# Kernel tuning notes

Hardware: AMD Instinct MI355X
Metric: run time of the kernel (lower is better)

The kernel has to match this reference:

```python
import jax, jax.numpy as jnp
import numpy as np

B, N, HID, NH = 8, 1024, 1024, 16
HD = HID // NH  # head_dim = 64
MLP = 4 * HID
EPS = 1e-6


def _xavier(key, fan_in, fan_out):
    lim = np.sqrt(6.0 / (fan_in + fan_out))
    return jax.random.uniform(key, (fan_in, fan_out), jnp.float32, -lim, lim)


def setup_inputs() -> dict:
    key = jax.random.key(0)
    ks = jax.random.split(key, 10)
    return {
        "x": jax.random.normal(ks[0], (B, N, HID), jnp.float32),
        "c": jax.random.normal(ks[1], (B, HID), jnp.float32),
        "w_ada": _xavier(ks[2], HID, 6 * HID), "b_ada": jnp.zeros((6 * HID,), jnp.float32),
        "wq": _xavier(ks[3], HID, HID), "bq": jnp.zeros((HID,), jnp.float32),
        "wk": _xavier(ks[4], HID, HID), "bk": jnp.zeros((HID,), jnp.float32),
        "wv": _xavier(ks[5], HID, HID), "bv": jnp.zeros((HID,), jnp.float32),
        "wo": _xavier(ks[6], HID, HID), "bo": jnp.zeros((HID,), jnp.float32),
        "w1": _xavier(ks[7], HID, MLP), "b1": jnp.zeros((MLP,), jnp.float32),
        "w2": _xavier(ks[8], MLP, HID), "b2": jnp.zeros((HID,), jnp.float32),
    }


def _ln(t):
    # LayerNorm, elementwise_affine=False, eps=1e-6
    mu = jnp.mean(t, axis=-1, keepdims=True)
    var = jnp.mean(jnp.square(t - mu), axis=-1, keepdims=True)
    return (t - mu) * jax.lax.rsqrt(var + EPS)


def _modulate(t, shift, scale):
    return t * (1.0 + scale[:, None, :]) + shift[:, None, :]


def reference(x, c, w_ada, b_ada, wq, bq, wk, bk, wv, bv, wo, bo, w1, b1, w2, b2):
    cmod = jax.nn.silu(c) @ w_ada + b_ada  # [B, 6*HID]
    sh_msa, sc_msa, g_msa, sh_mlp, sc_mlp, g_mlp = jnp.split(cmod, 6, axis=-1)

    xm = _modulate(_ln(x), sh_msa, sc_msa)  # [B, N, HID]
    q = (xm @ wq + bq).reshape(B, N, NH, HD)
    k = (xm @ wk + bk).reshape(B, N, NH, HD)
    v = (xm @ wv + bv).reshape(B, N, NH, HD)

    # NOTE: original scales by 1/head_dim (not 1/sqrt(head_dim)), fp32 softmax
    scores = jnp.einsum('bihd,bjhd->bhij', q, k) / HD
    attn = jax.nn.softmax(scores.astype(jnp.float32), axis=-1)
    out = jnp.einsum('bhij,bjhd->bihd', attn, v).astype(v.dtype)
    out = out.reshape(B, N, HID) @ wo + bo

    x = x + g_msa[:, None, :] * out

    xm2 = _modulate(_ln(x), sh_mlp, sc_mlp)
    h = jax.nn.gelu(xm2 @ w1 + b1, approximate=False)  # nn.GELU default = exact
    mlp_out = h @ w2 + b2
    return x + g_mlp[:, None, :] * mlp_out
```

## Files before the change

kernel.cpp:

```cpp
#include <hip/hip_runtime.h>
#include <hip/hip_bf16.h>
#include <cstdint>


typedef __bf16 bf16;
typedef __attribute__((ext_vector_type(8))) __bf16 bf16x8;
typedef __attribute__((ext_vector_type(4))) __bf16 bf16x4;
typedef __attribute__((ext_vector_type(4))) float f32x4;
typedef __attribute__((ext_vector_type(16))) float f32x16;

#define SEQ   1024
#define NHID  1024
#define NHEAD 16
#define HDIM  64
#define CMS   6144

#define GLD16(gp, lp)                                                  \
  __builtin_amdgcn_global_load_lds(                                    \
      (const __attribute__((address_space(1))) void*)(gp),             \
      (__attribute__((address_space(3))) void*)(lp), 16, 0, 0)

struct TP4 { const float* s[4]; bf16* d[4]; };

__global__ __launch_bounds__(256) void transpose_conv4(TP4 p)
{
  __shared__ float tile[32][33];
  const float* __restrict__ src = p.s[blockIdx.z];
  bf16* __restrict__ dst = p.d[blockIdx.z];
  int n0 = blockIdx.x * 32, k0 = blockIdx.y * 32;
  int tx = threadIdx.x & 31, ty = threadIdx.x >> 5;
#pragma unroll
  for (int i = 0; i < 32; i += 8)
    tile[ty + i][tx] = src[(size_t)(k0 + ty + i) * 1024 + n0 + tx];
  __syncthreads();
#pragma unroll
  for (int i = 0; i < 32; i += 8)
    dst[(size_t)(n0 + ty + i) * 1024 + k0 + tx] = (bf16)tile[tx][ty + i];
}

__global__ __launch_bounds__(256) void transpose_conv(
    const float* __restrict__ src, bf16* __restrict__ dst, int K, int N)
{
  __shared__ float tile[32][33];
  int n0 = blockIdx.x * 32, k0 = blockIdx.y * 32;
  int tx = threadIdx.x & 31, ty = threadIdx.x >> 5;
#pragma unroll
  for (int i = 0; i < 32; i += 8)
    tile[ty + i][tx] = src[(size_t)(k0 + ty + i) * N + n0 + tx];
  __syncthreads();
#pragma unroll
  for (int i = 0; i < 32; i += 8)
    dst[(size_t)(n0 + ty + i) * K + k0 + tx] = (bf16)tile[tx][ty + i];
}

__global__ __launch_bounds__(256) void ada_kernel(
    const float* __restrict__ c, const float* __restrict__ w_ada,
    const float* __restrict__ b_ada, float* __restrict__ cmod)
{
  __shared__ float cs[1024];
  int b = blockIdx.y;
  int col = blockIdx.x * 256 + threadIdx.x;
  for (int i = threadIdx.x; i < 1024; i += 256) {
    float cv = c[b * 1024 + i];
    cs[i] = cv / (1.0f + __expf(-cv));
  }
  __syncthreads();
  float acc = b_ada[col];
#pragma unroll 8
  for (int kk = 0; kk < 1024; kk++)
    acc += cs[kk] * w_ada[(size_t)kk * CMS + col];
  cmod[b * CMS + col] = acc;
}

__global__ __launch_bounds__(256) void ln_mod(
    const float* __restrict__ x, const float* __restrict__ cmod,
    bf16* __restrict__ out, int sh_off, int sc_off)
{
  int row = blockIdx.x, b = row >> 10, tid = threadIdx.x;
  const float4* xr = (const float4*)(x + (size_t)row * NHID);
  float4 v = xr[tid];
  float s  = v.x + v.y + v.z + v.w;
  float s2 = v.x * v.x + v.y * v.y + v.z * v.z + v.w * v.w;
#pragma unroll
  for (int off = 32; off; off >>= 1) {
    s  += __shfl_xor(s, off);
    s2 += __shfl_xor(s2, off);
  }
  __shared__ float red1[4], red2[4];
  int wave = tid >> 6, lane = tid & 63;
  if (lane == 0) { red1[wave] = s; red2[wave] = s2; }
  __syncthreads();
  float S  = red1[0] + red1[1] + red1[2] + red1[3];
  float S2 = red2[0] + red2[1] + red2[2] + red2[3];
  float mean = S * (1.0f / NHID);
  float var  = S2 * (1.0f / NHID) - mean * mean;
  float rs   = rsqrtf(var + 1e-6f);
  const float4* shp = (const float4*)(cmod + b * CMS + sh_off);
  const float4* scp = (const float4*)(cmod + b * CMS + sc_off);
  float4 sh4 = shp[tid], sc4 = scp[tid];
  bf16x4 o4;
  o4[0] = (bf16)((v.x - mean) * rs * (1.0f + sc4.x) + sh4.x);
  o4[1] = (bf16)((v.y - mean) * rs * (1.0f + sc4.y) + sh4.y);
  o4[2] = (bf16)((v.z - mean) * rs * (1.0f + sc4.z) + sh4.z);
  o4[3] = (bf16)((v.w - mean) * rs * (1.0f + sc4.w) + sh4.w);
  *(bf16x4*)(out + (size_t)row * NHID + tid * 4) = o4;
}

template <int EPI>
__global__ __launch_bounds__(256) void gemm_bt(
    const bf16* __restrict__ A, const bf16* __restrict__ Bt,
    const float* __restrict__ bias, const float* __restrict__ bias2,
    const float* __restrict__ bias3,
    bf16* __restrict__ outb, bf16* __restrict__ outb2,
    bf16* __restrict__ outb3, float* __restrict__ outf,
    const float* __restrict__ cmod, int gate_off,
    const float* __restrict__ resid,
    int N, int K)
{
  __shared__ __align__(16) bf16 As[128 * 64];
  __shared__ __align__(16) bf16 Bs[128 * 64];
  const int tid = threadIdx.x;
  const int bm = blockIdx.y * 128, bn = blockIdx.x * 128;

  const int wave = tid >> 6, lane = tid & 63;
  const int l32 = lane & 31, half = lane >> 5;
  const int wm = (wave >> 1) * 64, wn = (wave & 1) * 64;

  const int sr = tid >> 3;
  const int sc = tid & 7;

  f32x16 acc[2][2];
#pragma unroll
  for (int i = 0; i < 2; i++)
#pragma unroll
    for (int j = 0; j < 2; j++) acc[i][j] = (f32x16)0.0f;

  for (int k0 = 0; k0 < K; k0 += 64) {
#pragma unroll
    for (int i = 0; i < 4; i++) {
      int r = i * 32 + sr;
      int cg = (sc ^ (r & 7)) * 8;
      bf16* lbase_a = As + (size_t)(i * 256 + (tid & 192)) * 8;
      bf16* lbase_b = Bs + (size_t)(i * 256 + (tid & 192)) * 8;
      GLD16(A  + (size_t)(bm + r) * K + k0 + cg, lbase_a);
      GLD16(Bt + (size_t)(bn + r) * K + k0 + cg, lbase_b);
    }
    __syncthreads();
#pragma unroll
    for (int kk = 0; kk < 4; kk++) {
      int cc = kk * 2 + half;
      bf16x8 af[2], bfr[2];
#pragma unroll
      for (int t = 0; t < 2; t++) {
        int ra = wm + t * 32 + l32;
        int rb = wn + t * 32 + l32;
        af[t]  = *(const bf16x8*)(As + ra * 64 + ((cc ^ (ra & 7)) * 8));
        bfr[t] = *(const bf16x8*)(Bs + rb * 64 + ((cc ^ (rb & 7)) * 8));
      }
#pragma unroll
      for (int mt = 0; mt < 2; mt++)
#pragma unroll
        for (int nt = 0; nt < 2; nt++)
          acc[mt][nt] = __builtin_amdgcn_mfma_f32_32x32x16_bf16(
              af[mt], bfr[nt], acc[mt][nt], 0, 0, 0);
    }
    __syncthreads();
  }

  const int sel = bn >> 10;
  const float* bp = (EPI == 5)
      ? ((sel == 0) ? bias : (sel == 1) ? bias2 : bias3) : bias;
  bf16* qk_out = (EPI == 5) ? ((sel == 0) ? outb : outb2) : outb;

#pragma unroll
  for (int mt = 0; mt < 2; mt++) {
#pragma unroll
    for (int nt = 0; nt < 2; nt++) {
      int col = bn + wn + nt * 32 + l32;
      int colq = col & 1023;
      float bcol = (EPI == 5) ? bp[colq] : bias[col];
#pragma unroll
      for (int g = 0; g < 4; g++) {
        int row0 = bm + wm + mt * 32 + g * 8 + half * 4;
        if (EPI == 5 && sel == 2) {
          bf16x4 o4;
#pragma unroll
          for (int r = 0; r < 4; r++)
            o4[r] = (bf16)(acc[mt][nt][g * 4 + r] + bcol);
          int bb = row0 >> 10;
          *(bf16x4*)(outb3 + ((size_t)bb * NHID + colq) * SEQ +
                     (row0 & 1023)) = o4;
        } else if (EPI == 5) {
#pragma unroll
          for (int r = 0; r < 4; r++)
            qk_out[(size_t)(row0 + r) * 1024 + colq] =
                (bf16)(acc[mt][nt][g * 4 + r] + bcol);
        } else {
#pragma unroll
          for (int r = 0; r < 4; r++) {
            int row = row0 + r;
            float val = acc[mt][nt][g * 4 + r] + bcol;
            if (EPI == 1 || EPI == 3) {
              int bb = row >> 10;
              float gg = cmod[bb * CMS + gate_off + col];
              outf[(size_t)row * N + col] =
                  resid[(size_t)row * N + col] + gg * val;
            } else {
              float u2 = 2.0f * val * (0.7978845608f +
                                       0.0356774081f * val * val);
              float e = __expf(u2);
              float th = 1.0f - 2.0f / (e + 1.0f);
              outb[(size_t)row * N + col] = (bf16)(0.5f * val * (1.0f + th));
            }
          }
        }
      }
    }
  }
}

__global__ __launch_bounds__(256) void attn_mfma(
    const bf16* __restrict__ q, const bf16* __restrict__ k,
    const bf16* __restrict__ vt, bf16* __restrict__ o)
{
  __shared__ __align__(16) bf16 Ks[64 * 64];
  __shared__ __align__(16) bf16 Vs[64 * 64];
  __shared__ __align__(16) bf16 Ps[4][32 * 72];

  int bid = blockIdx.x;
  int qt = bid & 7, h = (bid >> 3) & 15, b = bid >> 7;
  int tid = threadIdx.x, wave = tid >> 6, lane = tid & 63;
  int quad = lane >> 4, l16 = lane & 15;
  int qbase = qt * 128 + wave * 32;

  bf16x8 qf[2][2];
  const bf16* qp = q + ((size_t)(b * SEQ + qbase)) * NHID + h * HDIM;
#pragma unroll
  for (int nt = 0; nt < 2; nt++)
#pragma unroll
    for (int kk = 0; kk < 2; kk++) {
      bf16x8 t = *(const bf16x8*)(qp + (size_t)(nt * 16 + l16) * NHID +
                                  kk * 32 + quad * 8);
#pragma unroll
      for (int j = 0; j < 8; j++) t[j] = (bf16)((float)t[j] * 0.015625f);
      qf[nt][kk] = t;
    }

  f32x4 oacc[4][2];
#pragma unroll
  for (int mt = 0; mt < 4; mt++)
#pragma unroll
    for (int nt = 0; nt < 2; nt++) oacc[mt][nt] = (f32x4)0.0f;
  float m_[2] = {-3.0e38f, -3.0e38f}, l_[2] = {0.0f, 0.0f};

  const bf16* kb = k + ((size_t)(b * SEQ)) * NHID + h * HDIM;
  const bf16* vb = vt + ((size_t)(b * NHID + h * HDIM)) * SEQ;

  const int sr0 = tid >> 3, sc0 = tid & 7;

  for (int kt = 0; kt < 16; kt++) {
    __syncthreads();
#pragma unroll
    for (int i = 0; i < 2; i++) {
      int r = i * 32 + sr0;
      int cg = (sc0 ^ (r & 7)) * 8;
      bf16* lk = Ks + (size_t)(i * 256 + (tid & 192)) * 8;
      bf16* lv = Vs + (size_t)(i * 256 + (tid & 192)) * 8;
      GLD16(kb + (size_t)(kt * 64 + r) * NHID + cg, lk);
      GLD16(vb + (size_t)r * SEQ + kt * 64 + cg, lv);
    }
    __syncthreads();

    f32x4 sacc[4][2];
#pragma unroll
    for (int mt = 0; mt < 4; mt++)
#pragma unroll
      for (int nt = 0; nt < 2; nt++) sacc[mt][nt] = (f32x4)0.0f;
#pragma unroll
    for (int kk = 0; kk < 2; kk++) {
      bf16x8 kf[4];
#pragma unroll
      for (int mt = 0; mt < 4; mt++) {
        int row = mt * 16 + l16;
        kf[mt] = *(const bf16x8*)(Ks + row * 64 +
                                  (((kk * 4 + quad) ^ (row & 7)) * 8));
      }
#pragma unroll
      for (int mt = 0; mt < 4; mt++)
#pragma unroll
        for (int nt = 0; nt < 2; nt++)
          sacc[mt][nt] = __builtin_amdgcn_mfma_f32_16x16x32_bf16(
              kf[mt], qf[nt][kk], sacc[mt][nt], 0, 0, 0);
    }

    float alpha[2];
#pragma unroll
    for (int nt = 0; nt < 2; nt++) {
      float tm = -3.0e38f;
#pragma unroll
      for (int mt = 0; mt < 4; mt++)
#pragma unroll
        for (int r = 0; r < 4; r++) tm = fmaxf(tm, sacc[mt][nt][r]);
      tm = fmaxf(tm, __shfl_xor(tm, 16));
      tm = fmaxf(tm, __shfl_xor(tm, 32));
      float mn = fmaxf(m_[nt], tm);
      alpha[nt] = __expf(m_[nt] - mn);
      m_[nt] = mn;
      float ts = 0.0f;
#pragma unroll
      for (int mt = 0; mt < 4; mt++) {
        bf16x4 pv;
#pragma unroll
        for (int r = 0; r < 4; r++) {
          float p = __expf(sacc[mt][nt][r] - mn);
          ts += p;
          pv[r] = (bf16)p;
        }
        *(bf16x4*)(&Ps[wave][(nt * 16 + l16) * 72 + mt * 16 + quad * 4]) = pv;
      }
      ts += __shfl_xor(ts, 16);
      ts += __shfl_xor(ts, 32);
      l_[nt] = l_[nt] * alpha[nt] + ts;
    }
#pragma unroll
    for (int mt = 0; mt < 4; mt++)
#pragma unroll
      for (int nt = 0; nt < 2; nt++)
#pragma unroll
        for (int r = 0; r < 4; r++) oacc[mt][nt][r] *= alpha[nt];

    __asm__ volatile("s_waitcnt lgkmcnt(0)" ::: "memory");

#pragma unroll
    for (int kk = 0; kk < 2; kk++) {
      bf16x8 vf[4], pf[2];
#pragma unroll
      for (int mt = 0; mt < 4; mt++) {
        int row = mt * 16 + l16;
        vf[mt] = *(const bf16x8*)(Vs + row * 64 +
                                  (((kk * 4 + quad) ^ (row & 7)) * 8));
      }
#pragma unroll
      for (int nt = 0; nt < 2; nt++)
        pf[nt] = *(const bf16x8*)(&Ps[wave][(nt * 16 + l16) * 72 +
                                            kk * 32 + quad * 8]);
#pragma unroll
      for (int mt = 0; mt < 4; mt++)
#pragma unroll
        for (int nt = 0; nt < 2; nt++)
          oacc[mt][nt] = __builtin_amdgcn_mfma_f32_16x16x32_bf16(
              vf[mt], pf[nt], oacc[mt][nt], 0, 0, 0);
    }
  }

#pragma unroll
  for (int nt = 0; nt < 2; nt++) {
    float rl = 1.0f / l_[nt];
#pragma unroll
    for (int mt = 0; mt < 4; mt++) {
      bf16x4 o4;
#pragma unroll
      for (int r = 0; r < 4; r++) o4[r] = (bf16)(oacc[mt][nt][r] * rl);
      *(bf16x4*)(o + ((size_t)(b * SEQ + qbase + nt * 16 + l16)) * NHID +
                 h * HDIM + mt * 16 + quad * 4) = o4;
    }
  }
}

#define OFF_CMOD 0u
#define OFF_WQT  196608u
#define OFF_WKT  (OFF_WQT + 2097152u)
#define OFF_WVT  (OFF_WKT + 2097152u)
#define OFF_WOT  (OFF_WVT + 2097152u)
#define OFF_W1T  (OFF_WOT + 2097152u)
#define OFF_W2T  (OFF_W1T + 8388608u)
#define OFF_X2   (OFF_W2T + 8388608u)
#define OFF_XM2  (OFF_X2  + 33554432u)
#define OFF_POOL (OFF_XM2 + 16777216u)

extern "C" void kernel_launch(void* const* d_in, const int* in_sizes, int n_in,
                              void* d_out, int out_size, void* d_ws, size_t ws_size,
                              hipStream_t stream)
{
  const float* x     = (const float*)d_in[0];
  const float* c     = (const float*)d_in[1];
  const float* w_ada = (const float*)d_in[2];
  const float* b_ada = (const float*)d_in[3];
  const float* wq = (const float*)d_in[4];  const float* bq = (const float*)d_in[5];
  const float* wk = (const float*)d_in[6];  const float* bk = (const float*)d_in[7];
  const float* wv = (const float*)d_in[8];  const float* bv = (const float*)d_in[9];
  const float* wo = (const float*)d_in[10]; const float* bo = (const float*)d_in[11];
  const float* w1 = (const float*)d_in[12]; const float* b1 = (const float*)d_in[13];
  const float* w2 = (const float*)d_in[14]; const float* b2 = (const float*)d_in[15];
  float* out = (float*)d_out;
  char* ws = (char*)d_ws;

  float* cmod = (float*)(ws + OFF_CMOD);
  bf16* wqT = (bf16*)(ws + OFF_WQT);
  bf16* wkT = (bf16*)(ws + OFF_WKT);
  bf16* wvT = (bf16*)(ws + OFF_WVT);
  bf16* woT = (bf16*)(ws + OFF_WOT);
  bf16* w1T = (bf16*)(ws + OFF_W1T);
  bf16* w2T = (bf16*)(ws + OFF_W2T);
  float* x2 = (float*)(ws + OFF_X2);
  bf16* xm2 = (bf16*)(ws + OFF_XM2);
  bf16* xm  = (bf16*)(ws + OFF_POOL);
  bf16* qb  = (bf16*)(ws + OFF_POOL + 16777216u);
  bf16* kb  = (bf16*)(ws + OFF_POOL + 33554432u);
  bf16* vtb = (bf16*)(ws + OFF_POOL + 50331648u);
  bf16* ob  = xm;
  bf16* hb  = xm;

  TP4 tp;
  tp.s[0] = wq; tp.s[1] = wk; tp.s[2] = wv; tp.s[3] = wo;
  tp.d[0] = wqT; tp.d[1] = wkT; tp.d[2] = wvT; tp.d[3] = woT;
  transpose_conv4<<<dim3(32, 32, 4), 256, 0, stream>>>(tp);
  transpose_conv<<<dim3(128, 32), 256, 0, stream>>>(w1, w1T, 1024, 4096);
  transpose_conv<<<dim3(32, 128), 256, 0, stream>>>(w2, w2T, 4096, 1024);

  ada_kernel<<<dim3(24, 8), 256, 0, stream>>>(c, w_ada, b_ada, cmod);

  ln_mod<<<8192, 256, 0, stream>>>(x, cmod, xm, 0, 1024);

  gemm_bt<5><<<dim3(24, 64), 256, 0, stream>>>(
      xm, wqT, bq, bk, bv, qb, kb, vtb, nullptr, nullptr, 0, nullptr,
      1024, 1024);

  attn_mfma<<<1024, 256, 0, stream>>>(qb, kb, vtb, ob);

  gemm_bt<1><<<dim3(8, 64), 256, 0, stream>>>(
      ob, woT, bo, nullptr, nullptr, nullptr, nullptr, nullptr, x2,
      cmod, 2048, x, 1024, 1024);

  ln_mod<<<8192, 256, 0, stream>>>(x2, cmod, xm2, 3072, 4096);

  gemm_bt<2><<<dim3(32, 64), 256, 0, stream>>>(
      xm2, w1T, b1, nullptr, nullptr, hb, nullptr, nullptr, nullptr,
      nullptr, 0, nullptr, 4096, 1024);

  gemm_bt<3><<<dim3(8, 64), 256, 0, stream>>>(
      hb, w2T, b2, nullptr, nullptr, nullptr, nullptr, nullptr, out,
      cmod, 5120, x2, 1024, 4096);
}
```

Measured before the change: 597.3 us.

## Replace GEMM with 8-wave double-buffered 256-row tiles and async prefetch pipeline

The simple single-buffered 128x128 GEMM is replaced by a 512-thread kernel with 256xBN tiles (BN=256 for the MLP up-projection). Operands are double-buffered in dynamic LDS, and the global-to-LDS loads for the next k-tile are interleaved across eight compute phases using explicit vmcnt waits and raw barriers. It also switches to 16x16x32 MFMA with setprio around the math. The goal is to hide memory latency and raise per-block reuse, at the cost of large LDS use (up to 128KB), which limits occupancy, and fragile hand-coded wait counts.

```diff
diff --git a/kernel.cpp b/kernel.cpp
--- a/kernel.cpp
+++ b/kernel.cpp
@@ -7,7 +7,6 @@
 typedef __attribute__((ext_vector_type(8))) __bf16 bf16x8;
 typedef __attribute__((ext_vector_type(4))) __bf16 bf16x4;
 typedef __attribute__((ext_vector_type(4))) float f32x4;
-typedef __attribute__((ext_vector_type(16))) float f32x16;
 
 #define SEQ   1024
 #define NHID  1024
@@ -19,6 +18,14 @@
   __builtin_amdgcn_global_load_lds(                                    \
       (const __attribute__((address_space(1))) void*)(gp),             \
       (__attribute__((address_space(3))) void*)(lp), 16, 0, 0)
+
+template <int N> __device__ __forceinline__ void vmwait() {
+  if constexpr (N == 0)      asm volatile("s_waitcnt vmcnt(0)" ::: "memory");
+  else if constexpr (N == 3) asm volatile("s_waitcnt vmcnt(3)" ::: "memory");
+  else if constexpr (N == 4) asm volatile("s_waitcnt vmcnt(4)" ::: "memory");
+  else if constexpr (N == 6) asm volatile("s_waitcnt vmcnt(6)" ::: "memory");
+  else                       asm volatile("s_waitcnt vmcnt(8)" ::: "memory");
+}
 
 struct TP4 { const float* s[4]; bf16* d[4]; };
 
@@ -106,8 +113,8 @@
   *(bf16x4*)(out + (size_t)row * NHID + tid * 4) = o4;
 }
 
-template <int EPI>
-__global__ __launch_bounds__(256) void gemm_bt(
+template <int EPI, int BN>
+__global__ __launch_bounds__(512, 2) void gemm8(
     const bf16* __restrict__ A, const bf16* __restrict__ Bt,
     const float* __restrict__ bias, const float* __restrict__ bias2,
     const float* __restrict__ bias3,
@@ -117,103 +124,165 @@
     const float* __restrict__ resid,
     int N, int K)
 {
-  __shared__ __align__(16) bf16 As[128 * 64];
-  __shared__ __align__(16) bf16 Bs[128 * 64];
-  const int tid = threadIdx.x;
-  const int bm = blockIdx.y * 128, bn = blockIdx.x * 128;
-
+  constexpr int BNH   = BN / 2;
+  constexpr int LB    = BNH / 64;
+  constexpr int NF    = BN / 128;
+  constexpr int VMS   = 4 + 2 * LB;
+  constexpr int VMF   = 2 + LB;
+  constexpr int BOFF  = 65536;
+  constexpr int BBUF  = BNH * 256;
+  constexpr int BHALF = BNH * 128;
+
+  extern __shared__ __align__(16) char smem[];
+
+  const int tid  = threadIdx.x;
+  const int bm = blockIdx.y * 256, bn = blockIdx.x * BN;
   const int wave = tid >> 6, lane = tid & 63;
-  const int l32 = lane & 31, half = lane >> 5;
-  const int wm = (wave >> 1) * 64, wn = (wave & 1) * 64;
-
-  const int sr = tid >> 3;
-  const int sc = tid & 7;
-
-  f32x16 acc[2][2];
-#pragma unroll
-  for (int i = 0; i < 2; i++)
-#pragma unroll
-    for (int j = 0; j < 2; j++) acc[i][j] = (f32x16)0.0f;
-
-  for (int k0 = 0; k0 < K; k0 += 64) {
-#pragma unroll
-    for (int i = 0; i < 4; i++) {
-      int r = i * 32 + sr;
-      int cg = (sc ^ (r & 7)) * 8;
-      bf16* lbase_a = As + (size_t)(i * 256 + (tid & 192)) * 8;
-      bf16* lbase_b = Bs + (size_t)(i * 256 + (tid & 192)) * 8;
-      GLD16(A  + (size_t)(bm + r) * K + k0 + cg, lbase_a);
-      GLD16(Bt + (size_t)(bn + r) * K + k0 + cg, lbase_b);
-    }
-    __syncthreads();
-#pragma unroll
-    for (int kk = 0; kk < 4; kk++) {
-      int cc = kk * 2 + half;
-      bf16x8 af[2], bfr[2];
-#pragma unroll
-      for (int t = 0; t < 2; t++) {
-        int ra = wm + t * 32 + l32;
-        int rb = wn + t * 32 + l32;
-        af[t]  = *(const bf16x8*)(As + ra * 64 + ((cc ^ (ra & 7)) * 8));
-        bfr[t] = *(const bf16x8*)(Bs + rb * 64 + ((cc ^ (rb & 7)) * 8));
+  const int wr = wave >> 2, wc = wave & 3;
+  const int l16 = lane & 15, q4 = lane >> 4;
+
+  const int rq = tid >> 3;
+  const int ch = ((tid & 7) ^ (rq & 7)) * 8;
+  const int wbase = (tid & 448) * 16;
+
+  const int aRowB = (wr * 64 + l16) * 128;
+  const int bRowB = (wc * (BN >> 3) + l16) * 128;
+  const int slotB = (q4 ^ (l16 & 7)) * 16;
+
+  f32x4 acc[2][2][4][NF];
+#pragma unroll
+  for (int a0 = 0; a0 < 2; a0++)
+#pragma unroll
+    for (int a1 = 0; a1 < 2; a1++)
+#pragma unroll
+      for (int a2 = 0; a2 < 4; a2++)
+#pragma unroll
+        for (int a3 = 0; a3 < NF; a3++) acc[a0][a1][a2][a3] = (f32x4)0.0f;
+
+  auto stA = [&](int buf, int half, int T) {
+    const bf16* g = A + (size_t)(bm + half * 128 + rq) * K + T * 64 + ch;
+    char* l = smem + buf * 32768 + half * 16384 + wbase;
+    GLD16(g, l);
+    GLD16(g + (size_t)64 * K, l + 8192);
+  };
+  auto stB = [&](int buf, int half, int T) {
+    const bf16* g = Bt + (size_t)(bn + half * BNH + rq) * K + T * 64 + ch;
+    char* l = smem + BOFF + buf * BBUF + half * BHALF + wbase;
+    GLD16(g, l);
+    if constexpr (LB == 2) { GLD16(g + (size_t)64 * K, l + 8192); }
+  };
+
+#define PHASE(VMN, BUF, QM, QN, ...)                                       \
+  {                                                                        \
+    vmwait<VMN>();                                                         \
+    __builtin_amdgcn_s_barrier();                                          \
+    asm volatile("" ::: "memory");                                         \
+    __VA_ARGS__                                                            \
+    const char* ab = smem + (BUF) * 32768 + (QM) * 16384 + aRowB;          \
+    const char* bb = smem + BOFF + (BUF) * BBUF + (QN) * BHALF + bRowB;    \
+    bf16x8 afr[2][4]; bf16x8 bfr[2][NF];                                   \
+    _Pragma("unroll")                                                      \
+    for (int ks = 0; ks < 2; ks++) {                                       \
+      const int sb = slotB ^ (ks * 64);                                    \
+      _Pragma("unroll")                                                    \
+      for (int mf = 0; mf < 4; mf++)                                       \
+        afr[ks][mf] = *(const bf16x8*)(ab + mf * 2048 + sb);               \
+      _Pragma("unroll")                                                    \
+      for (int nf = 0; nf < NF; nf++)                                      \
+        bfr[ks][nf] = *(const bf16x8*)(bb + nf * 2048 + sb);               \
+    }                                                                      \
+    __builtin_amdgcn_s_setprio(1);                                         \
+    _Pragma("unroll")                                                      \
+    for (int mf = 0; mf < 4; mf++)                                         \
+      _Pragma("unroll")                                                    \
+      for (int nf = 0; nf < NF; nf++) {                                    \
+        acc[QM][QN][mf][nf] = __builtin_amdgcn_mfma_f32_16x16x32_bf16(     \
+            afr[0][mf], bfr[0][nf], acc[QM][QN][mf][nf], 0, 0, 0);         \
+        acc[QM][QN][mf][nf] = __builtin_amdgcn_mfma_f32_16x16x32_bf16(     \
+            afr[1][mf], bfr[1][nf], acc[QM][QN][mf][nf], 0, 0, 0);         \
+      }                                                                    \
+    __builtin_amdgcn_s_setprio(0);                                         \
+  }
+
+  const int NT = K >> 6, NI = NT >> 1;
+
+  stA(0, 0, 0); stB(0, 0, 0);
+  stA(0, 1, 0); stB(0, 1, 0);
+  stA(1, 0, 1); stB(1, 0, 1);
+
+  for (int i = 0; i < NI - 1; ++i) {
+    const int t = 2 * i;
+    PHASE(VMS, 0, 0, 0, stA(1, 1, t + 1); stB(1, 1, t + 1);)
+    PHASE(VMS, 0, 0, 1, ;)
+    PHASE(VMS, 0, 1, 0, stA(0, 0, t + 2);)
+    PHASE(VMS, 0, 1, 1, stB(0, 0, t + 2);)
+    PHASE(VMS, 1, 0, 0, stA(0, 1, t + 2); stB(0, 1, t + 2);)
+    PHASE(VMS, 1, 0, 1, ;)
+    PHASE(VMS, 1, 1, 0, stA(1, 0, t + 3);)
+    PHASE(VMS, 1, 1, 1, stB(1, 0, t + 3);)
+  }
+  {
+    const int t = NT - 2;
+    PHASE(VMS, 0, 0, 0, stA(1, 1, t + 1); stB(1, 1, t + 1);)
+    PHASE(VMS, 0, 0, 1, ;)
+    PHASE(VMS, 0, 1, 0, ;)
+    PHASE(VMS, 0, 1, 1, ;)
+    PHASE(VMF, 1, 0, 0, ;)
+    PHASE(0,   1, 0, 1, ;)
+    PHASE(0,   1, 1, 0, ;)
+    PHASE(0,   1, 1, 1, ;)
+  }
+#undef PHASE
+
+  const int colBase = bn + wc * (BN >> 3) + l16;
+  const int rowBase = bm + wr * 64 + q4 * 4;
+#pragma unroll
+  for (int qm = 0; qm < 2; qm++)
+#pragma unroll
+  for (int qn = 0; qn < 2; qn++)
+#pragma unroll
+  for (int mf = 0; mf < 4; mf++)
+#pragma unroll
+  for (int nf = 0; nf < NF; nf++) {
+    const int col  = colBase + qn * BNH + nf * 16;
+    const int row0 = rowBase + qm * 128 + mf * 16;
+    f32x4 v = acc[qm][qn][mf][nf];
+    if constexpr (EPI == 5) {
+      const int sel = bn >> 10;
+      const float* bp = (sel == 0) ? bias : (sel == 1) ? bias2 : bias3;
+      const int colq = col & 1023;
+      const float bcol = bp[colq];
+      if (sel == 2) {
+        bf16x4 o4;
+#pragma unroll
+        for (int r = 0; r < 4; r++) o4[r] = (bf16)(v[r] + bcol);
+        const int bidx = row0 >> 10;
+        *(bf16x4*)(outb3 + ((size_t)bidx * NHID + colq) * SEQ +
+                   (row0 & 1023)) = o4;
+      } else {
+        bf16* qk = (sel == 0) ? outb : outb2;
+#pragma unroll
+        for (int r = 0; r < 4; r++)
+          qk[(size_t)(row0 + r) * 1024 + colq] = (bf16)(v[r] + bcol);
       }
-#pragma unroll
-      for (int mt = 0; mt < 2; mt++)
-#pragma unroll
-        for (int nt = 0; nt < 2; nt++)
-          acc[mt][nt] = __builtin_amdgcn_mfma_f32_32x32x16_bf16(
-              af[mt], bfr[nt], acc[mt][nt], 0, 0, 0);
-    }
-    __syncthreads();
-  }
-
-  const int sel = bn >> 10;
-  const float* bp = (EPI == 5)
-      ? ((sel == 0) ? bias : (sel == 1) ? bias2 : bias3) : bias;
-  bf16* qk_out = (EPI == 5) ? ((sel == 0) ? outb : outb2) : outb;
-
-#pragma unroll
-  for (int mt = 0; mt < 2; mt++) {
-#pragma unroll
-    for (int nt = 0; nt < 2; nt++) {
-      int col = bn + wn + nt * 32 + l32;
-      int colq = col & 1023;
-      float bcol = (EPI == 5) ? bp[colq] : bias[col];
-#pragma unroll
-      for (int g = 0; g < 4; g++) {
-        int row0 = bm + wm + mt * 32 + g * 8 + half * 4;
-        if (EPI == 5 && sel == 2) {
-          bf16x4 o4;
-#pragma unroll
-          for (int r = 0; r < 4; r++)
-            o4[r] = (bf16)(acc[mt][nt][g * 4 + r] + bcol);
-          int bb = row0 >> 10;
-          *(bf16x4*)(outb3 + ((size_t)bb * NHID + colq) * SEQ +
-                     (row0 & 1023)) = o4;
-        } else if (EPI == 5) {
-#pragma unroll
-          for (int r = 0; r < 4; r++)
-            qk_out[(size_t)(row0 + r) * 1024 + colq] =
-                (bf16)(acc[mt][nt][g * 4 + r] + bcol);
-        } else {
-#pragma unroll
-          for (int r = 0; r < 4; r++) {
-            int row = row0 + r;
-            float val = acc[mt][nt][g * 4 + r] + bcol;
-            if (EPI == 1 || EPI == 3) {
-              int bb = row >> 10;
-              float gg = cmod[bb * CMS + gate_off + col];
-              outf[(size_t)row * N + col] =
-                  resid[(size_t)row * N + col] + gg * val;
-            } else {
-              float u2 = 2.0f * val * (0.7978845608f +
-                                       0.0356774081f * val * val);
-              float e = __expf(u2);
-              float th = 1.0f - 2.0f / (e + 1.0f);
-              outb[(size_t)row * N + col] = (bf16)(0.5f * val * (1.0f + th));
-            }
-          }
-        }
+    } else if constexpr (EPI == 2) {
+      const float bcol = bias[col];
+#pragma unroll
+      for (int r = 0; r < 4; r++) {
+        float val = v[r] + bcol;
+        float u2 = 2.0f * val * (0.7978845608f + 0.0356774081f * val * val);
+        float e = __expf(u2);
+        float th = 1.0f - 2.0f / (e + 1.0f);
+        outb[(size_t)(row0 + r) * N + col] = (bf16)(0.5f * val * (1.0f + th));
+      }
+    } else {
+      const float bcol = bias[col];
+#pragma unroll
+      for (int r = 0; r < 4; r++) {
+        const int row = row0 + r;
+        const float gg = cmod[(row >> 10) * CMS + gate_off + col];
+        outf[(size_t)row * N + col] =
+            resid[(size_t)row * N + col] + gg * (v[r] + bcol);
       }
     }
   }
@@ -411,6 +480,19 @@
   bf16* ob  = xm;
   bf16* hb  = xm;
 
+  static bool attr_set = false;
+  if (!attr_set) {
+    hipFuncSetAttribute(reinterpret_cast<const void*>(&gemm8<5, 128>),
+                        hipFuncAttributeMaxDynamicSharedMemorySize, 131072);
+    hipFuncSetAttribute(reinterpret_cast<const void*>(&gemm8<1, 128>),
+                        hipFuncAttributeMaxDynamicSharedMemorySize, 131072);
+    hipFuncSetAttribute(reinterpret_cast<const void*>(&gemm8<2, 256>),
+                        hipFuncAttributeMaxDynamicSharedMemorySize, 131072);
+    hipFuncSetAttribute(reinterpret_cast<const void*>(&gemm8<3, 128>),
+                        hipFuncAttributeMaxDynamicSharedMemorySize, 131072);
+    attr_set = true;
+  }
+
   TP4 tp;
   tp.s[0] = wq; tp.s[1] = wk; tp.s[2] = wv; tp.s[3] = wo;
   tp.d[0] = wqT; tp.d[1] = wkT; tp.d[2] = wvT; tp.d[3] = woT;
@@ -422,23 +504,23 @@
 
   ln_mod<<<8192, 256, 0, stream>>>(x, cmod, xm, 0, 1024);
 
-  gemm_bt<5><<<dim3(24, 64), 256, 0, stream>>>(
+  gemm8<5, 128><<<dim3(24, 32), 512, 98304, stream>>>(
       xm, wqT, bq, bk, bv, qb, kb, vtb, nullptr, nullptr, 0, nullptr,
       1024, 1024);
 
   attn_mfma<<<1024, 256, 0, stream>>>(qb, kb, vtb, ob);
 
-  gemm_bt<1><<<dim3(8, 64), 256, 0, stream>>>(
+  gemm8<1, 128><<<dim3(8, 32), 512, 98304, stream>>>(
       ob, woT, bo, nullptr, nullptr, nullptr, nullptr, nullptr, x2,
       cmod, 2048, x, 1024, 1024);
 
   ln_mod<<<8192, 256, 0, stream>>>(x2, cmod, xm2, 3072, 4096);
 
-  gemm_bt<2><<<dim3(32, 64), 256, 0, stream>>>(
+  gemm8<2, 256><<<dim3(16, 32), 512, 131072, stream>>>(
       xm2, w1T, b1, nullptr, nullptr, hb, nullptr, nullptr, nullptr,
       nullptr, 0, nullptr, 4096, 1024);
 
-  gemm_bt<3><<<dim3(8, 64), 256, 0, stream>>>(
+  gemm8<3, 128><<<dim3(8, 32), 512, 98304, stream>>>(
       hb, w2T, b2, nullptr, nullptr, nullptr, nullptr, nullptr, out,
       cmod, 5120, x2, 1024, 4096);
 }
```

Result: slower. 616.6 us (+3.2%).

## Rewrite GEMM with double-buffered K=32 tiles, 16x16 MFMA and XCD-aware block mapping

Applied to the files above, without the earlier changes.

Replaces the single-buffered BK=64 GEMM with a double-buffered BK=32 pipeline, so the next tile's global-to-LDS loads are issued before the current tile's MFMAs and only one barrier is needed per iteration. The MFMA shape changes from 32x32x16 to 16x16x32 with 4x4 accumulator tiles per wave, and the launch bounds now request 4 blocks per CU. A 1-D grid is remapped so that consecutive row-blocks land on the same XCD, aiming to improve L2 reuse of the A and B tiles. The risks are more register pressure, the loss of the 32x32 instruction's throughput, and shorter K steps that expose barrier overhead.

```diff
diff --git a/kernel.cpp b/kernel.cpp
--- a/kernel.cpp
+++ b/kernel.cpp
@@ -7,7 +7,6 @@
 typedef __attribute__((ext_vector_type(8))) __bf16 bf16x8;
 typedef __attribute__((ext_vector_type(4))) __bf16 bf16x4;
 typedef __attribute__((ext_vector_type(4))) float f32x4;
-typedef __attribute__((ext_vector_type(16))) float f32x16;
 
 #define SEQ   1024
 #define NHID  1024
@@ -107,7 +106,7 @@
 }
 
 template <int EPI>
-__global__ __launch_bounds__(256) void gemm_bt(
+__global__ __launch_bounds__(256, 4) void gemm8(
     const bf16* __restrict__ A, const bf16* __restrict__ Bt,
     const float* __restrict__ bias, const float* __restrict__ bias2,
     const float* __restrict__ bias3,
@@ -117,103 +116,114 @@
     const float* __restrict__ resid,
     int N, int K)
 {
-  __shared__ __align__(16) bf16 As[128 * 64];
-  __shared__ __align__(16) bf16 Bs[128 * 64];
-  const int tid = threadIdx.x;
-  const int bm = blockIdx.y * 128, bn = blockIdx.x * 128;
+  __shared__ __align__(16) char smem[32768];
+
+  const int tid  = threadIdx.x;
+  const int xcd  = blockIdx.x & 7;
+  const int slot = blockIdx.x >> 3;
+  const int by   = xcd * 8 + (slot & 7);
+  const int bx   = slot >> 3;
+  const int bm = by * 128, bn = bx * 128;
 
   const int wave = tid >> 6, lane = tid & 63;
-  const int l32 = lane & 31, half = lane >> 5;
-  const int wm = (wave >> 1) * 64, wn = (wave & 1) * 64;
-
-  const int sr = tid >> 3;
-  const int sc = tid & 7;
-
-  f32x16 acc[2][2];
-#pragma unroll
-  for (int i = 0; i < 2; i++)
-#pragma unroll
-    for (int j = 0; j < 2; j++) acc[i][j] = (f32x16)0.0f;
-
-  for (int k0 = 0; k0 < K; k0 += 64) {
-#pragma unroll
-    for (int i = 0; i < 4; i++) {
-      int r = i * 32 + sr;
-      int cg = (sc ^ (r & 7)) * 8;
-      bf16* lbase_a = As + (size_t)(i * 256 + (tid & 192)) * 8;
-      bf16* lbase_b = Bs + (size_t)(i * 256 + (tid & 192)) * 8;
-      GLD16(A  + (size_t)(bm + r) * K + k0 + cg, lbase_a);
-      GLD16(Bt + (size_t)(bn + r) * K + k0 + cg, lbase_b);
-    }
+  const int wr = wave >> 1, wc = wave & 1;
+  const int l16 = lane & 15, q4 = lane >> 4;
+
+  const int rq = tid >> 2;
+  const int ch = ((tid & 3) ^ ((rq >> 1) & 3)) * 8;
+  const int wbase = (tid & 192) * 16;
+
+  const int slotB = (q4 ^ ((l16 >> 1) & 3)) * 16;
+  const int aRowB = (wr * 64 + l16) * 64 + slotB;
+  const int bRowB = (wc * 64 + l16) * 64 + slotB;
+
+  f32x4 acc[4][4];
+#pragma unroll
+  for (int i = 0; i < 4; i++)
+#pragma unroll
+    for (int j = 0; j < 4; j++) acc[i][j] = (f32x4)0.0f;
+
+  auto stage = [&](int buf, int T) {
+    const bf16* ga = A  + (size_t)(bm + rq) * K + T * 32 + ch;
+    const bf16* gb = Bt + (size_t)(bn + rq) * K + T * 32 + ch;
+    char* la = smem + buf * 8192 + wbase;
+    char* lb = smem + 16384 + buf * 8192 + wbase;
+    GLD16(ga, la);
+    GLD16(ga + (size_t)64 * K, la + 4096);
+    GLD16(gb, lb);
+    GLD16(gb + (size_t)64 * K, lb + 4096);
+  };
+
+  const int NT = K >> 5;
+
+  stage(0, 0);
+  __syncthreads();
+
+  bf16x8 afr[4], bfr[4];
+  for (int t = 0; t < NT; ++t) {
+    const int cur = t & 1;
+    if (t + 1 < NT) stage(cur ^ 1, t + 1);
+    const char* ab_ = smem + cur * 8192 + aRowB;
+    const char* bb_ = smem + 16384 + cur * 8192 + bRowB;
+#pragma unroll
+    for (int f = 0; f < 4; f++) {
+      afr[f] = *(const bf16x8*)(ab_ + f * 1024);
+      bfr[f] = *(const bf16x8*)(bb_ + f * 1024);
+    }
+#pragma unroll
+    for (int mf = 0; mf < 4; mf++)
+#pragma unroll
+      for (int nf = 0; nf < 4; nf++)
+        acc[mf][nf] = __builtin_amdgcn_mfma_f32_16x16x32_bf16(
+            afr[mf], bfr[nf], acc[mf][nf], 0, 0, 0);
     __syncthreads();
-#pragma unroll
-    for (int kk = 0; kk < 4; kk++) {
-      int cc = kk * 2 + half;
-      bf16x8 af[2], bfr[2];
-#pragma unroll
-      for (int t = 0; t < 2; t++) {
-        int ra = wm + t * 32 + l32;
-        int rb = wn + t * 32 + l32;
-        af[t]  = *(const bf16x8*)(As + ra * 64 + ((cc ^ (ra & 7)) * 8));
-        bfr[t] = *(const bf16x8*)(Bs + rb * 64 + ((cc ^ (rb & 7)) * 8));
-      }
-#pragma unroll
-      for (int mt = 0; mt < 2; mt++)
-#pragma unroll
-        for (int nt = 0; nt < 2; nt++)
-          acc[mt][nt] = __builtin_amdgcn_mfma_f32_32x32x16_bf16(
-              af[mt], bfr[nt], acc[mt][nt], 0, 0, 0);
-    }
-    __syncthreads();
-  }
-
-  const int sel = bn >> 10;
-  const float* bp = (EPI == 5)
-      ? ((sel == 0) ? bias : (sel == 1) ? bias2 : bias3) : bias;
-  bf16* qk_out = (EPI == 5) ? ((sel == 0) ? outb : outb2) : outb;
-
-#pragma unroll
-  for (int mt = 0; mt < 2; mt++) {
-#pragma unroll
-    for (int nt = 0; nt < 2; nt++) {
-      int col = bn + wn + nt * 32 + l32;
-      int colq = col & 1023;
-      float bcol = (EPI == 5) ? bp[colq] : bias[col];
-#pragma unroll
-      for (int g = 0; g < 4; g++) {
-        int row0 = bm + wm + mt * 32 + g * 8 + half * 4;
-        if (EPI == 5 && sel == 2) {
-          bf16x4 o4;
-#pragma unroll
-          for (int r = 0; r < 4; r++)
-            o4[r] = (bf16)(acc[mt][nt][g * 4 + r] + bcol);
-          int bb = row0 >> 10;
-          *(bf16x4*)(outb3 + ((size_t)bb * NHID + colq) * SEQ +
-                     (row0 & 1023)) = o4;
-        } else if (EPI == 5) {
-#pragma unroll
-          for (int r = 0; r < 4; r++)
-            qk_out[(size_t)(row0 + r) * 1024 + colq] =
-                (bf16)(acc[mt][nt][g * 4 + r] + bcol);
-        } else {
-#pragma unroll
-          for (int r = 0; r < 4; r++) {
-            int row = row0 + r;
-            float val = acc[mt][nt][g * 4 + r] + bcol;
-            if (EPI == 1 || EPI == 3) {
-              int bb = row >> 10;
-              float gg = cmod[bb * CMS + gate_off + col];
-              outf[(size_t)row * N + col] =
-                  resid[(size_t)row * N + col] + gg * val;
-            } else {
-              float u2 = 2.0f * val * (0.7978845608f +
-                                       0.0356774081f * val * val);
-              float e = __expf(u2);
-              float th = 1.0f - 2.0f / (e + 1.0f);
-              outb[(size_t)row * N + col] = (bf16)(0.5f * val * (1.0f + th));
-            }
-          }
-        }
+  }
+
+  const int colBase = bn + wc * 64 + l16;
+  const int rowBase = bm + wr * 64 + q4 * 4;
+#pragma unroll
+  for (int mf = 0; mf < 4; mf++)
+#pragma unroll
+  for (int nf = 0; nf < 4; nf++) {
+    const int col  = colBase + nf * 16;
+    const int row0 = rowBase + mf * 16;
+    f32x4 v = acc[mf][nf];
+    if constexpr (EPI == 5) {
+      const int sel = bn >> 10;
+      const float* bp = (sel == 0) ? bias : (sel == 1) ? bias2 : bias3;
+      const int colq = col & 1023;
+      const float bcol = bp[colq];
+      if (sel == 2) {
+        bf16x4 o4;
+#pragma unroll
+        for (int r = 0; r < 4; r++) o4[r] = (bf16)(v[r] + bcol);
+        const int bidx = row0 >> 10;
+        *(bf16x4*)(outb3 + ((size_t)bidx * NHID + colq) * SEQ +
+                   (row0 & 1023)) = o4;
+      } else {
+        bf16* qk = (sel == 0) ? outb : outb2;
+#pragma unroll
+        for (int r = 0; r < 4; r++)
+          qk[(size_t)(row0 + r) * 1024 + colq] = (bf16)(v[r] + bcol);
+      }
+    } else if constexpr (EPI == 2) {
+      const float bcol = bias[col];
+#pragma unroll
+      for (int r = 0; r < 4; r++) {
+        float val = v[r] + bcol;
+        float u2g = 2.0f * val * (0.7978845608f + 0.0356774081f * val * val);
+        float e = __expf(u2g);
+        float th = 1.0f - 2.0f / (e + 1.0f);
+        outb[(size_t)(row0 + r) * N + col] = (bf16)(0.5f * val * (1.0f + th));
+      }
+    } else {
+      const float bcol = bias[col];
+#pragma unroll
+      for (int r = 0; r < 4; r++) {
+        const int row = row0 + r;
+        const float gg = cmod[(row >> 10) * CMS + gate_off + col];
+        outf[(size_t)row * N + col] =
+            resid[(size_t)row * N + col] + gg * (v[r] + bcol);
       }
     }
   }
@@ -422,23 +432,23 @@
 
   ln_mod<<<8192, 256, 0, stream>>>(x, cmod, xm, 0, 1024);
 
-  gemm_bt<5><<<dim3(24, 64), 256, 0, stream>>>(
+  gemm8<5><<<1536, 256, 0, stream>>>(
       xm, wqT, bq, bk, bv, qb, kb, vtb, nullptr, nullptr, 0, nullptr,
       1024, 1024);
 
   attn_mfma<<<1024, 256, 0, stream>>>(qb, kb, vtb, ob);
 
-  gemm_bt<1><<<dim3(8, 64), 256, 0, stream>>>(
+  gemm8<1><<<512, 256, 0, stream>>>(
       ob, woT, bo, nullptr, nullptr, nullptr, nullptr, nullptr, x2,
       cmod, 2048, x, 1024, 1024);
 
   ln_mod<<<8192, 256, 0, stream>>>(x2, cmod, xm2, 3072, 4096);
 
-  gemm_bt<2><<<dim3(32, 64), 256, 0, stream>>>(
+  gemm8<2><<<2048, 256, 0, stream>>>(
       xm2, w1T, b1, nullptr, nullptr, hb, nullptr, nullptr, nullptr,
       nullptr, 0, nullptr, 4096, 1024);
 
-  gemm_bt<3><<<dim3(8, 64), 256, 0, stream>>>(
+  gemm8<3><<<512, 256, 0, stream>>>(
       hb, w2T, b2, nullptr, nullptr, nullptr, nullptr, nullptr, out,
       cmod, 5120, x2, 1024, 4096);
 }
```

Result: no change. 594.6 us (-0.5%).
